# Optimization experiments

Measured on AMD Instinct MI355X. Metric: run time of the kernel, lower is better.

Reference implementation:

```python
import jax, jax.numpy as jnp
import numpy as np

D_MODEL = 256
NHEAD = 8
DK = D_MODEL // NHEAD
EDGE_FEAT_DIM = 7
N_NODES = 2048
N_EDGES = 65536
LN_EPS = 1e-5


def _ln(x, g, b):
    mu = jnp.mean(x, axis=-1, keepdims=True)
    var = jnp.mean(jnp.square(x - mu), axis=-1, keepdims=True)
    return (x - mu) * jax.lax.rsqrt(var + LN_EPS) * g + b


def setup_inputs() -> dict:
    key = jax.random.key(0)
    ks = jax.random.split(key, 16)
    d, h2 = D_MODEL, 2 * D_MODEL
    s = 0.02
    inp = {
        "h": jax.random.normal(ks[0], (N_NODES, d), jnp.float32),
        "edge_attr": jax.random.normal(ks[1], (N_EDGES, EDGE_FEAT_DIM), jnp.float32),
        # weights stored as (in, out): y = x @ W + b (matches torch Linear math)
        "Wq": s * jax.random.normal(ks[2], (d, d), jnp.float32),
        "bq": jnp.zeros((d,), jnp.float32),
        "Wk": s * jax.random.normal(ks[3], (d, d), jnp.float32),
        "bk": jnp.zeros((d,), jnp.float32),
        "Wv": s * jax.random.normal(ks[4], (d, d), jnp.float32),
        "bv": jnp.zeros((d,), jnp.float32),
        "Wo": s * jax.random.normal(ks[5], (d, d), jnp.float32),
        "bo": jnp.zeros((d,), jnp.float32),
        "We": s * jax.random.normal(ks[6], (EDGE_FEAT_DIM, NHEAD), jnp.float32),
        "be": jnp.zeros((NHEAD,), jnp.float32),
        "ln1_g": jnp.ones((d,), jnp.float32),
        "ln1_b": jnp.zeros((d,), jnp.float32),
        "fln_g": jnp.ones((d,), jnp.float32),
        "fln_b": jnp.zeros((d,), jnp.float32),
        "W1": s * jax.random.normal(ks[7], (d, h2), jnp.float32),
        "b1": jnp.zeros((h2,), jnp.float32),
        "W2": s * jax.random.normal(ks[8], (h2, d), jnp.float32),
        "b2": jnp.zeros((d,), jnp.float32),
        "edge_index": jax.random.randint(ks[9], (2, N_EDGES), 0, N_NODES, jnp.int64 if jax.config.jax_enable_x64 else jnp.int32),
    }
    return inp


def reference(h, edge_attr, Wq, bq, Wk, bk, Wv, bv, Wo, bo, We, be,
              ln1_g, ln1_b, fln_g, fln_b, W1, b1, W2, b2, edge_index):
    N = h.shape[0]
    res = h
    # edge bias scattered into dense (N, N, H) tensor
    eb = edge_attr @ We + be                                  # (E, H)
    attn_bias = jnp.zeros((N, N, NHEAD), h.dtype).at[edge_index[0], edge_index[1]].set(eb)
    Q = (h @ Wq + bq).reshape(N, NHEAD, DK)
    K = (h @ Wk + bk).reshape(N, NHEAD, DK)
    V = (h @ Wv + bv).reshape(N, NHEAD, DK)
    scores = jnp.einsum('nhd,mhd->nmh', Q, K) / jnp.sqrt(jnp.float32(DK)) + attn_bias
    attn = jax.nn.softmax(scores, axis=1)                     # softmax over keys m
    out = jnp.einsum('nmh,mhd->nhd', attn, V).reshape(N, D_MODEL)
    out = out @ Wo + bo
    h1 = _ln(res + out, ln1_g, ln1_b)
    ffn = jax.nn.gelu(_ln(h1, fln_g, fln_b) @ W1 + b1, approximate=False) @ W2 + b2
    return h1 + ffn
```

## Files before the change

### kernel.cpp

```cpp
#include <hip/hip_runtime.h>
#include <math.h>

#define NN 2048
#define NE 65536
#define DM 256
#define NH 8
#define DKH 32
#define CAP 128
#define TM2 128
#define SPLIT 4

typedef __attribute__((ext_vector_type(8))) short bf16x8;
typedef __attribute__((ext_vector_type(4))) float f32x4;

#define WAVE_LDS_SYNC() __asm__ volatile("s_waitcnt lgkmcnt(0)" ::: "memory")

__device__ __forceinline__ unsigned short f2b(float f) {
    unsigned u = __float_as_uint(f);
    unsigned r = (u + 0x7FFFu + ((u >> 16) & 1u)) >> 16;
    return (unsigned short)r;
}
__device__ __forceinline__ float b2f(unsigned short s) {
    return __uint_as_float(((unsigned)s) << 16);
}
__device__ __forceinline__ unsigned pk2(float a, float b) {
    unsigned ua = __float_as_uint(a) + 0x8000u;
    unsigned ub = __float_as_uint(b) + 0x8000u;
    return (ua >> 16) | (ub & 0xFFFF0000u);
}

__global__ __launch_bounds__(256) void prep_all_kernel(
    const float* __restrict__ Wq, const float* __restrict__ Wk,
    const float* __restrict__ Wv, const float* __restrict__ Wo,
    const float* __restrict__ W1, const float* __restrict__ W2,
    const float* __restrict__ ea, const float* __restrict__ We,
    const float* __restrict__ be, const int* __restrict__ ei,
    unsigned short* __restrict__ Wqkvt, unsigned short* __restrict__ Wot,
    unsigned short* __restrict__ W1t, unsigned short* __restrict__ W2t,
    float* __restrict__ eb, int* __restrict__ cnt, int* __restrict__ lst)
{
    int b = blockIdx.x;
    if (b < 2048) {
        int i = b * 256 + threadIdx.x;
        if (i < 196608) {
            int n = i >> 8, k = i & 255;
            const float* W = (n < 256) ? Wq : (n < 512) ? Wk : Wv;
            Wqkvt[i] = f2b(W[k * 256 + (n & 255)]);
        } else if (i < 262144) {
            int j = i - 196608;
            int n = j >> 8, k = j & 255;
            Wot[j] = f2b(Wo[k * 256 + n]);
        } else if (i < 393216) {
            int j = i - 262144;
            int n = j >> 8, k = j & 255;
            W1t[j] = f2b(W1[(size_t)k * 512 + n]);
        } else {
            int j = i - 393216;
            int n = j >> 9, k = j & 511;
            W2t[j] = f2b(W2[(size_t)k * 256 + n]);
        }
    } else {
        int e = (b - 2048) * 256 + threadIdx.x;
        float acc[NH];
#pragma unroll
        for (int hh = 0; hh < NH; ++hh) acc[hh] = be[hh];
#pragma unroll
        for (int f = 0; f < 7; ++f) {
            float x = ea[e * 7 + f];
#pragma unroll
            for (int hh = 0; hh < NH; ++hh) acc[hh] = fmaf(x, We[f * NH + hh], acc[hh]);
        }
#pragma unroll
        for (int hh = 0; hh < NH; ++hh)
            eb[e * NH + hh] = acc[hh] * 1.44269504088896f;
        int s = ei[e];
        int p = atomicAdd(&cnt[s], 1);
        if (p < CAP) lst[s * CAP + p] = e;
    }
}

__global__ __launch_bounds__(128) void rowprep_kernel(
    const int* __restrict__ ei, const int* __restrict__ cnt,
    const int* __restrict__ lst, int* __restrict__ sortedDest,
    int* __restrict__ sortedE, int* __restrict__ rowOff)
{
    __shared__ int ds[CAP], es[CAP];
    __shared__ int bc[16], off[17];
    int n = blockIdx.x, t = threadIdx.x;
    int c = cnt[n]; if (c > CAP) c = CAP;
    if (t < 16) bc[t] = 0;
    int e = -1, d = -1;
    if (t < c) { e = lst[n * CAP + t]; d = ei[NE + e]; }
    ds[t] = d; es[t] = e;
    __syncthreads();
    bool win = (t < c);
    if (win) {
        for (int j = 0; j < c; ++j)
            if (ds[j] == d && es[j] > e) { win = false; break; }
    }
    int bkt = (d >= 0) ? (d >> 7) : 0;
    int pos = -1;
    if (win) pos = atomicAdd(&bc[bkt], 1);
    __syncthreads();
    if (t == 0) {
        int s = 0;
        for (int i = 0; i < 16; ++i) { off[i] = s; s += bc[i]; }
        off[16] = s;
    }
    __syncthreads();
    if (win) {
        int p = off[bkt] + pos;
        sortedDest[n * CAP + p] = d;
        sortedE[n * CAP + p] = e;
    }
    if (t < 17) rowOff[n * 17 + t] = off[t];
}

template <int EPI, int MT, int AF32>
__global__ __launch_bounds__(MT * 4) void gemm_bf16(
    const void* __restrict__ Av, const unsigned short* __restrict__ Bt,
    const float* __restrict__ bias0, const float* __restrict__ bias1,
    const float* __restrict__ bias2, const float* __restrict__ resid,
    void* __restrict__ out0, void* __restrict__ out1, void* __restrict__ out2,
    int M, int N, int K)
{
    __shared__ __align__(16) unsigned short As[MT][136];
    __shared__ __align__(16) unsigned short Bs[64][136];
    int tid = threadIdx.x;
    int wv = tid >> 6, l = tid & 63, l15 = l & 15, quad = l >> 4;
    int m0 = blockIdx.y * MT, n0 = blockIdx.x * 64;

    f32x4 acc[4];
#pragma unroll
    for (int i = 0; i < 4; ++i) acc[i] = (f32x4){0.f, 0.f, 0.f, 0.f};

    for (int k0 = 0; k0 < K; k0 += 128) {
        if (MT == 64) {
            int row = tid >> 2, cb = (tid & 3) * 32;
            if (AF32) {
                const float* ap = (const float*)Av + (size_t)(m0 + row) * K + k0 + cb;
#pragma unroll
                for (int i = 0; i < 4; ++i) {
                    float4 f0 = *(const float4*)(ap + i * 8);
                    float4 f1 = *(const float4*)(ap + i * 8 + 4);
                    uint4 pk = { pk2(f0.x, f0.y), pk2(f0.z, f0.w),
                                 pk2(f1.x, f1.y), pk2(f1.z, f1.w) };
                    *(uint4*)&As[row][cb + i * 8] = pk;
                }
            } else {
                const unsigned short* ap =
                    (const unsigned short*)Av + (size_t)(m0 + row) * K + k0 + cb;
#pragma unroll
                for (int i = 0; i < 4; ++i)
                    *(uint4*)&As[row][cb + i * 8] = *(const uint4*)(ap + i * 8);
            }
            const unsigned short* bp = Bt + (size_t)(n0 + row) * K + k0 + cb;
#pragma unroll
            for (int i = 0; i < 4; ++i)
                *(uint4*)&Bs[row][cb + i * 8] = *(const uint4*)(bp + i * 8);
        } else {
            int rowa = tid >> 2, cba = (tid & 3) * 32;
            const unsigned short* ap =
                (const unsigned short*)Av + (size_t)(m0 + rowa) * K + k0 + cba;
#pragma unroll
            for (int i = 0; i < 4; ++i)
                *(uint4*)&As[rowa][cba + i * 8] = *(const uint4*)(ap + i * 8);
            int rowb = tid >> 1, cbb = (tid & 1) * 64;
            const unsigned short* bp = Bt + (size_t)(n0 + rowb) * K + k0 + cbb;
#pragma unroll
            for (int i = 0; i < 8; ++i)
                *(uint4*)&Bs[rowb][cbb + i * 8] = *(const uint4*)(bp + i * 8);
        }
        __syncthreads();
#pragma unroll
        for (int ks = 0; ks < 4; ++ks) {
            bf16x8 a = *(const bf16x8*)&As[wv * 16 + l15][ks * 32 + quad * 8];
#pragma unroll
            for (int nt = 0; nt < 4; ++nt) {
                bf16x8 b = *(const bf16x8*)&Bs[nt * 16 + l15][ks * 32 + quad * 8];
                acc[nt] = __builtin_amdgcn_mfma_f32_16x16x32_bf16(a, b, acc[nt], 0, 0, 0);
            }
        }
        __syncthreads();
    }

#pragma unroll
    for (int nt = 0; nt < 4; ++nt) {
        int colb = n0 + nt * 16;
        if (EPI == 2 && colb >= 512) {
            int n = colb + l15 - 512;
            float bv = bias2[n];
            uint2 pk = { pk2(acc[nt][0] + bv, acc[nt][1] + bv),
                         pk2(acc[nt][2] + bv, acc[nt][3] + bv) };
            *(uint2*)((unsigned short*)out2 + (size_t)n * NN + m0 + wv * 16 + quad * 4) = pk;
            continue;
        }
#pragma unroll
        for (int r = 0; r < 4; ++r) {
            int row = m0 + wv * 16 + quad * 4 + r;
            int col = colb + l15;
            float v = acc[nt][r];
            if (EPI == 0) {
                v += bias0[col];
                if (resid) v += resid[(size_t)row * N + col];
                ((float*)out0)[(size_t)row * N + col] = v;
            } else if (EPI == 1) {
                v += bias0[col];
                v = 0.5f * v * (1.0f + erff(v * 0.70710678118654752f));
                ((unsigned short*)out0)[(size_t)row * N + col] = f2b(v);
            } else {
                if (col < 256) {
                    v = (v + bias0[col]) * 0.2550348592f;
                    ((unsigned short*)out0)[(size_t)row * 256 + col] = f2b(v);
                } else {
                    v += bias1[col - 256];
                    ((unsigned short*)out1)[(size_t)row * 256 + col - 256] = f2b(v);
                }
            }
        }
    }
}

__global__ __launch_bounds__(256) void attn_mfma(
    const unsigned short* __restrict__ Qb, const unsigned short* __restrict__ Kb,
    const unsigned short* __restrict__ Vt, const float* __restrict__ eb,
    const int* __restrict__ sortedDest, const int* __restrict__ sortedE,
    const int* __restrict__ rowOff,
    float* __restrict__ accD, float* __restrict__ lD)
{
    __shared__ __align__(16) unsigned short Ks[TM2][40];
    __shared__ __align__(16) unsigned short Vs[32][TM2 + 8];
    __shared__ __align__(16) unsigned short Pn[4][16][TM2 + 16];
    int h = blockIdx.y, tid = threadIdx.x;
    int wv = tid >> 6, l = tid & 63, l15 = l & 15, quad = l >> 4;
    int n0 = blockIdx.x * 64 + wv * 16;
    int mz = blockIdx.z;

    bf16x8 aq = *(const bf16x8*)(Qb + (size_t)(n0 + l15) * DM + h * 32 + quad * 8);

    f32x4 oacc[2];
    oacc[0] = (f32x4){0.f, 0.f, 0.f, 0.f};
    oacc[1] = (f32x4){0.f, 0.f, 0.f, 0.f};
    float lacc = 0.f;
    float dreg = 0.f;
    const unsigned short* Vth = Vt + (size_t)h * 32 * NN;

    int r16 = l >> 2, sub = l & 3;
    int frow = n0 + r16;

    for (int t = 0; t < NN / (TM2 * SPLIT); ++t) {
        int m0 = (mz * (NN / SPLIT)) + t * TM2;
        int ti = m0 >> 7;
        {
            int r = tid >> 1, kc = (tid & 1) * 16;
            const unsigned short* ks = Kb + (size_t)(m0 + r) * DM + h * 32 + kc;
            *(uint4*)&Ks[r][kc]     = *(const uint4*)(ks);
            *(uint4*)&Ks[r][kc + 8] = *(const uint4*)(ks + 8);
            int d = tid >> 3, mc = (tid & 7) * 16;
            const unsigned short* vs = Vth + (size_t)d * NN + m0 + mc;
            *(uint4*)&Vs[d][mc]     = *(const uint4*)(vs);
            *(uint4*)&Vs[d][mc + 8] = *(const uint4*)(vs + 8);
        }
        __syncthreads();
#pragma unroll
        for (int mt = 0; mt < TM2 / 16; ++mt) {
            bf16x8 ak = *(const bf16x8*)&Ks[mt * 16 + l15][quad * 8];
            f32x4 s = __builtin_amdgcn_mfma_f32_16x16x32_bf16(
                ak, aq, (f32x4){0.f, 0.f, 0.f, 0.f}, 0, 0, 0);
            float p0 = __builtin_amdgcn_exp2f(s[0]);
            float p1 = __builtin_amdgcn_exp2f(s[1]);
            float p2 = __builtin_amdgcn_exp2f(s[2]);
            float p3 = __builtin_amdgcn_exp2f(s[3]);
            lacc += (p0 + p1) + (p2 + p3);
            *(uint2*)&Pn[wv][l15][mt * 16 + quad * 4] =
                (uint2){pk2(p0, p1), pk2(p2, p3)};
        }
        WAVE_LDS_SYNC();
        {
            int o0 = rowOff[frow * 17 + ti];
            int o1 = rowOff[frow * 17 + ti + 1];
            for (int idx = o0 + sub; idx < o1; idx += 4) {
                int d = sortedDest[frow * CAP + idx] - m0;
                int e = sortedE[frow * CAP + idx];
                float expb = __builtin_amdgcn_exp2f(eb[e * NH + h]);
                float pold = b2f(Pn[wv][r16][d]);
                Pn[wv][r16][d] = f2b(pold * expb);
                dreg += pold * (expb - 1.0f);
            }
        }
        WAVE_LDS_SYNC();
#pragma unroll
        for (int kc = 0; kc < TM2 / 32; ++kc) {
            bf16x8 ap = *(const bf16x8*)&Pn[wv][l15][kc * 32 + quad * 8];
#pragma unroll
            for (int nt = 0; nt < 2; ++nt) {
                bf16x8 bv = *(const bf16x8*)&Vs[nt * 16 + l15][kc * 32 + quad * 8];
                oacc[nt] = __builtin_amdgcn_mfma_f32_16x16x32_bf16(ap, bv, oacc[nt], 0, 0, 0);
            }
        }
        __syncthreads();
    }

    lacc += __shfl_xor(lacc, 16);
    lacc += __shfl_xor(lacc, 32);
    dreg += __shfl_xor(dreg, 1);
    dreg += __shfl_xor(dreg, 2);
    float dtot = __shfl(dreg, l15 * 4);
    float* lDp = lD + (size_t)mz * NN * NH;
    if (l < 16)
        lDp[(size_t)(n0 + l) * NH + h] = lacc + dtot;
    float* aDp = accD + (size_t)mz * NN * DM;
#pragma unroll
    for (int nt = 0; nt < 2; ++nt)
#pragma unroll
        for (int r = 0; r < 4; ++r)
            aDp[(size_t)(n0 + quad * 4 + r) * DM + h * 32 + nt * 16 + l15] = oacc[nt][r];
}

__global__ __launch_bounds__(512) void tail_fused_kernel(
    const float* __restrict__ accD, const float* __restrict__ lD,
    const unsigned short* __restrict__ Wot, const float* __restrict__ bo,
    const float* __restrict__ h, const float* __restrict__ ln1g,
    const float* __restrict__ ln1b, const float* __restrict__ flng,
    const float* __restrict__ flnb,
    const unsigned short* __restrict__ W1t, const float* __restrict__ fb1,
    const unsigned short* __restrict__ W2t, const float* __restrict__ fb2,
    float* __restrict__ out)
{
    __shared__ float linv[16][8];
    __shared__ __align__(16) unsigned short As[16][264];
    __shared__ float Tt[16][264];
    __shared__ __align__(16) unsigned short X2s[16][264];
    __shared__ __align__(16) unsigned short F1s[16][520];
    int tid = threadIdx.x, m0 = blockIdx.x * 16;
    int wv = tid >> 6, l = tid & 63, l15 = l & 15, quad = l >> 4;

    if (tid < 128) {
        int r = tid >> 3, hh = tid & 7;
        float ls = 0.f;
#pragma unroll
        for (int s = 0; s < SPLIT; ++s)
            ls += lD[(size_t)s * NN * NH + (size_t)(m0 + r) * NH + hh];
        linv[r][hh] = 1.0f / ls;
    }
    __syncthreads();
    {
        int col = tid & 255, rh = tid >> 8;
#pragma unroll
        for (int ch = 0; ch < 8; ++ch) {
            int row = ch * 2 + rh;
            float o = 0.f;
#pragma unroll
            for (int s = 0; s < SPLIT; ++s)
                o += accD[(size_t)s * NN * DM + (size_t)(m0 + row) * DM + col];
            As[row][col] = f2b(o * linv[row][col >> 5]);
        }
    }
    __syncthreads();

    f32x4 acc[2];
    acc[0] = (f32x4){0.f, 0.f, 0.f, 0.f};
    acc[1] = (f32x4){0.f, 0.f, 0.f, 0.f};
#pragma unroll
    for (int k0 = 0; k0 < 256; k0 += 32) {
        bf16x8 a = *(const bf16x8*)&As[l15][k0 + quad * 8];
#pragma unroll
        for (int nt = 0; nt < 2; ++nt) {
            int row = wv * 32 + nt * 16 + l15;
            bf16x8 b = *(const bf16x8*)(Wot + (size_t)row * 256 + k0 + quad * 8);
            acc[nt] = __builtin_amdgcn_mfma_f32_16x16x32_bf16(a, b, acc[nt], 0, 0, 0);
        }
    }
#pragma unroll
    for (int nt = 0; nt < 2; ++nt)
#pragma unroll
        for (int r = 0; r < 4; ++r) {
            int row = quad * 4 + r, col = wv * 32 + nt * 16 + l15;
            Tt[row][col] = acc[nt][r] + bo[col] + h[(size_t)(m0 + row) * DM + col];
        }
    __syncthreads();

    if (tid < 256) {
        int rr = tid >> 4, l16 = tid & 15;
        float x[16];
#pragma unroll
        for (int j = 0; j < 16; ++j) x[j] = Tt[rr][l16 + 16 * j];
        float mu = 0.f;
#pragma unroll
        for (int j = 0; j < 16; ++j) mu += x[j];
#pragma unroll
        for (int off = 1; off < 16; off <<= 1) mu += __shfl_xor(mu, off);
        mu *= (1.0f / 256.0f);
        float var = 0.f;
#pragma unroll
        for (int j = 0; j < 16; ++j) { float d = x[j] - mu; var += d * d; }
#pragma unroll
        for (int off = 1; off < 16; off <<= 1) var += __shfl_xor(var, off);
        float rs = rsqrtf(var * (1.0f / 256.0f) + 1e-5f);
        float y[16]; float mu2 = 0.f;
#pragma unroll
        for (int j = 0; j < 16; ++j) {
            int c = l16 + 16 * j;
            y[j] = (x[j] - mu) * rs * ln1g[c] + ln1b[c];
            mu2 += y[j];
        }
#pragma unroll
        for (int off = 1; off < 16; off <<= 1) mu2 += __shfl_xor(mu2, off);
        mu2 *= (1.0f / 256.0f);
        float var2 = 0.f;
#pragma unroll
        for (int j = 0; j < 16; ++j) { float d = y[j] - mu2; var2 += d * d; }
#pragma unroll
        for (int off = 1; off < 16; off <<= 1) var2 += __shfl_xor(var2, off);
        float rs2 = rsqrtf(var2 * (1.0f / 256.0f) + 1e-5f);
#pragma unroll
        for (int j = 0; j < 16; ++j) {
            int c = l16 + 16 * j;
            Tt[rr][c] = y[j];
            X2s[rr][c] = f2b((y[j] - mu2) * rs2 * flng[c] + flnb[c]);
        }
    }
    __syncthreads();

    f32x4 acc1[4];
#pragma unroll
    for (int i = 0; i < 4; ++i) acc1[i] = (f32x4){0.f, 0.f, 0.f, 0.f};
#pragma unroll
    for (int k0 = 0; k0 < 256; k0 += 32) {
        bf16x8 a = *(const bf16x8*)&X2s[l15][k0 + quad * 8];
#pragma unroll
        for (int nt = 0; nt < 4; ++nt) {
            int row = wv * 64 + nt * 16 + l15;
            bf16x8 b = *(const bf16x8*)(W1t + (size_t)row * 256 + k0 + quad * 8);
            acc1[nt] = __builtin_amdgcn_mfma_f32_16x16x32_bf16(a, b, acc1[nt], 0, 0, 0);
        }
    }
#pragma unroll
    for (int nt = 0; nt < 4; ++nt)
#pragma unroll
        for (int r = 0; r < 4; ++r) {
            int row = quad * 4 + r, col = wv * 64 + nt * 16 + l15;
            float v = acc1[nt][r] + fb1[col];
            v = 0.5f * v * (1.0f + erff(v * 0.70710678118654752f));
            F1s[row][col] = f2b(v);
        }
    __syncthreads();

    f32x4 acc2[2];
    acc2[0] = (f32x4){0.f, 0.f, 0.f, 0.f};
    acc2[1] = (f32x4){0.f, 0.f, 0.f, 0.f};
#pragma unroll
    for (int k0 = 0; k0 < 512; k0 += 32) {
        bf16x8 a = *(const bf16x8*)&F1s[l15][k0 + quad * 8];
#pragma unroll
        for (int nt = 0; nt < 2; ++nt) {
            int row = wv * 32 + nt * 16 + l15;
            bf16x8 b = *(const bf16x8*)(W2t + (size_t)row * 512 + k0 + quad * 8);
            acc2[nt] = __builtin_amdgcn_mfma_f32_16x16x32_bf16(a, b, acc2[nt], 0, 0, 0);
        }
    }
#pragma unroll
    for (int nt = 0; nt < 2; ++nt)
#pragma unroll
        for (int r = 0; r < 4; ++r) {
            int row = quad * 4 + r, col = wv * 32 + nt * 16 + l15;
            out[(size_t)(m0 + row) * DM + col] = acc2[nt][r] + fb2[col] + Tt[row][col];
        }
}

extern "C" void kernel_launch(void* const* d_in, const int* in_sizes, int n_in,
                              void* d_out, int out_size, void* d_ws, size_t ws_size,
                              hipStream_t stream)
{
    const float* h    = (const float*)d_in[0];
    const float* ea   = (const float*)d_in[1];
    const float* Wq   = (const float*)d_in[2];
    const float* bq   = (const float*)d_in[3];
    const float* Wk   = (const float*)d_in[4];
    const float* bk   = (const float*)d_in[5];
    const float* Wv   = (const float*)d_in[6];
    const float* bv   = (const float*)d_in[7];
    const float* Wo   = (const float*)d_in[8];
    const float* bo   = (const float*)d_in[9];
    const float* We   = (const float*)d_in[10];
    const float* be   = (const float*)d_in[11];
    const float* ln1g = (const float*)d_in[12];
    const float* ln1b = (const float*)d_in[13];
    const float* flng = (const float*)d_in[14];
    const float* flnb = (const float*)d_in[15];
    const float* W1   = (const float*)d_in[16];
    const float* b1   = (const float*)d_in[17];
    const float* W2   = (const float*)d_in[18];
    const float* b2   = (const float*)d_in[19];
    const int*   ei   = (const int*)d_in[20];
    float* out = (float*)d_out;

    char* p = (char*)d_ws;
    float* eb   = (float*)p;           p += (size_t)NE * NH * 4;
    int*   cnt  = (int*)p;             p += (size_t)NN * 4;
    int*   lst  = (int*)p;             p += (size_t)NN * CAP * 4;
    int*   sD   = (int*)p;             p += (size_t)NN * CAP * 4;
    int*   sE   = (int*)p;             p += (size_t)NN * CAP * 4;
    int*   rOff = (int*)p;             p += (size_t)NN * 17 * 4;
    unsigned short* Wqkvt = (unsigned short*)p; p += (size_t)768 * 256 * 2;
    unsigned short* Wot   = (unsigned short*)p; p += (size_t)256 * 256 * 2;
    unsigned short* W1t   = (unsigned short*)p; p += (size_t)512 * 256 * 2;
    unsigned short* W2t   = (unsigned short*)p; p += (size_t)256 * 512 * 2;
    unsigned short* Qb    = (unsigned short*)p; p += (size_t)NN * DM * 2;
    unsigned short* Kb    = (unsigned short*)p; p += (size_t)NN * DM * 2;
    unsigned short* Vt    = (unsigned short*)p; p += (size_t)NN * DM * 2;
    float* accD = (float*)p;           p += (size_t)SPLIT * NN * DM * 4;
    float* lD   = (float*)p;           p += (size_t)SPLIT * NN * NH * 4;

    hipMemsetAsync(cnt, 0, (size_t)NN * 4, stream);
    prep_all_kernel<<<2048 + NE / 256, 256, 0, stream>>>(
        Wq, Wk, Wv, Wo, W1, W2, ea, We, be, ei,
        Wqkvt, Wot, W1t, W2t, eb, cnt, lst);
    rowprep_kernel<<<NN, 128, 0, stream>>>(ei, cnt, lst, sD, sE, rOff);

    gemm_bf16<2, 64, 1><<<dim3(768 / 64, NN / 64), 256, 0, stream>>>(
        h, Wqkvt, bq, bk, bv, nullptr, Qb, Kb, Vt, NN, 768, 256);

    attn_mfma<<<dim3(NN / 64, NH, SPLIT), 256, 0, stream>>>(
        Qb, Kb, Vt, eb, sD, sE, rOff, accD, lD);

    tail_fused_kernel<<<NN / 16, 512, 0, stream>>>(
        accD, lD, Wot, bo, h, ln1g, ln1b, flng, flnb,
        W1t, b1, W2t, b2, out);
}
```

Measured before the change: 173.8 us.

## Tile weight transposes via LDS, pre-convert h to bf16, head-major Q/K layout

Weight transposition in the prep kernel moves from one-element-per-thread strided reads to 64x64 LDS-tiled transposes, cutting the block count and making the global accesses coalesced. The prep kernel also converts h to bf16 once, so the QKV GEMM reads bf16 input (template flag changed) instead of converting fp32 itself. Q and K are written in head-major [head][node][32] layout, so the attention kernel loads contiguous 64-byte rows per head instead of strided slices of 512-byte rows. This adds a workspace buffer and relies on the GEMM variant with flag 0 accepting bf16 input correctly.

Result: faster. 166.7 us (-4.1%).

```diff
diff --git a/kernel.cpp b/kernel.cpp
--- a/kernel.cpp
+++ b/kernel.cpp
@@ -29,38 +29,69 @@
     return (ua >> 16) | (ub & 0xFFFF0000u);
 }
 
+__device__ __forceinline__ void transpose_tile(
+    const float* __restrict__ src, int srcStride, int nc0, int k0s,
+    unsigned short* __restrict__ dst, int dstK, int n0d, int tid)
+{
+    __shared__ unsigned short T[64][66];
+    int tx = tid & 63, ty = tid >> 6;
+#pragma unroll
+    for (int r = 0; r < 16; ++r) {
+        int kk = ty + r * 4;
+        T[tx][kk] = f2b(src[(size_t)(k0s + kk) * srcStride + nc0 + tx]);
+    }
+    __syncthreads();
+#pragma unroll
+    for (int r = 0; r < 16; ++r) {
+        int nn = ty + r * 4;
+        dst[(size_t)(n0d + nn) * dstK + k0s + tx] = T[nn][tx];
+    }
+}
+
 __global__ __launch_bounds__(256) void prep_all_kernel(
     const float* __restrict__ Wq, const float* __restrict__ Wk,
     const float* __restrict__ Wv, const float* __restrict__ Wo,
     const float* __restrict__ W1, const float* __restrict__ W2,
-    const float* __restrict__ ea, const float* __restrict__ We,
-    const float* __restrict__ be, const int* __restrict__ ei,
+    const float* __restrict__ h, const float* __restrict__ ea,
+    const float* __restrict__ We, const float* __restrict__ be,
+    const int* __restrict__ ei,
     unsigned short* __restrict__ Wqkvt, unsigned short* __restrict__ Wot,
     unsigned short* __restrict__ W1t, unsigned short* __restrict__ W2t,
+    unsigned short* __restrict__ hb,
     float* __restrict__ eb, int* __restrict__ cnt, int* __restrict__ lst)
 {
     int b = blockIdx.x;
-    if (b < 2048) {
-        int i = b * 256 + threadIdx.x;
-        if (i < 196608) {
-            int n = i >> 8, k = i & 255;
-            const float* W = (n < 256) ? Wq : (n < 512) ? Wk : Wv;
-            Wqkvt[i] = f2b(W[k * 256 + (n & 255)]);
-        } else if (i < 262144) {
-            int j = i - 196608;
-            int n = j >> 8, k = j & 255;
-            Wot[j] = f2b(Wo[k * 256 + n]);
-        } else if (i < 393216) {
-            int j = i - 262144;
-            int n = j >> 8, k = j & 255;
-            W1t[j] = f2b(W1[(size_t)k * 512 + n]);
+    if (b < 128) {
+        const float* src; int srcStride, nc0, k0s, dstK, n0d;
+        unsigned short* dst;
+        if (b < 48) {
+            int tn = b >> 2, tk = b & 3, n0 = tn * 64;
+            src = (n0 < 256) ? Wq : (n0 < 512) ? Wk : Wv;
+            srcStride = 256; nc0 = n0 & 255; k0s = tk * 64;
+            dst = Wqkvt; dstK = 256; n0d = n0;
+        } else if (b < 64) {
+            int t = b - 48, tn = t >> 2, tk = t & 3;
+            src = Wo; srcStride = 256; nc0 = tn * 64; k0s = tk * 64;
+            dst = Wot; dstK = 256; n0d = tn * 64;
+        } else if (b < 96) {
+            int t = b - 64, tn = t >> 2, tk = t & 3;
+            src = W1; srcStride = 512; nc0 = tn * 64; k0s = tk * 64;
+            dst = W1t; dstK = 256; n0d = tn * 64;
         } else {
-            int j = i - 393216;
-            int n = j >> 9, k = j & 511;
-            W2t[j] = f2b(W2[(size_t)k * 256 + n]);
-        }
+            int t = b - 96, tn = t >> 3, tk = t & 7;
+            src = W2; srcStride = 256; nc0 = tn * 64; k0s = tk * 64;
+            dst = W2t; dstK = 512; n0d = tn * 64;
+        }
+        transpose_tile(src, srcStride, nc0, k0s, dst, dstK, n0d, threadIdx.x);
+    } else if (b < 384) {
+        int j = ((b - 128) * 256 + threadIdx.x) * 8;
+        const float* hp = h + j;
+        float4 f0 = *(const float4*)hp, f1 = *(const float4*)(hp + 4);
+        uint4 pk = { pk2(f0.x, f0.y), pk2(f0.z, f0.w),
+                     pk2(f1.x, f1.y), pk2(f1.z, f1.w) };
+        *(uint4*)(hb + j) = pk;
     } else {
-        int e = (b - 2048) * 256 + threadIdx.x;
+        int e = (b - 384) * 256 + threadIdx.x;
         float acc[NH];
 #pragma unroll
         for (int hh = 0; hh < NH; ++hh) acc[hh] = be[hh];
@@ -211,10 +242,13 @@
             } else {
                 if (col < 256) {
                     v = (v + bias0[col]) * 0.2550348592f;
-                    ((unsigned short*)out0)[(size_t)row * 256 + col] = f2b(v);
+                    ((unsigned short*)out0)[(size_t)(col >> 5) * (NN * 32)
+                        + (size_t)row * 32 + (col & 31)] = f2b(v);
                 } else {
-                    v += bias1[col - 256];
-                    ((unsigned short*)out1)[(size_t)row * 256 + col - 256] = f2b(v);
+                    int kc = col - 256;
+                    v += bias1[kc];
+                    ((unsigned short*)out1)[(size_t)(kc >> 5) * (NN * 32)
+                        + (size_t)row * 32 + (kc & 31)] = f2b(v);
                 }
             }
         }
@@ -236,7 +270,9 @@
     int n0 = blockIdx.x * 64 + wv * 16;
     int mz = blockIdx.z;
 
-    bf16x8 aq = *(const bf16x8*)(Qb + (size_t)(n0 + l15) * DM + h * 32 + quad * 8);
+    const unsigned short* Qh = Qb + (size_t)h * NN * 32;
+    const unsigned short* Kh = Kb + (size_t)h * NN * 32;
+    bf16x8 aq = *(const bf16x8*)(Qh + (size_t)(n0 + l15) * 32 + quad * 8);
 
     f32x4 oacc[2];
     oacc[0] = (f32x4){0.f, 0.f, 0.f, 0.f};
@@ -253,7 +289,7 @@
         int ti = m0 >> 7;
         {
             int r = tid >> 1, kc = (tid & 1) * 16;
-            const unsigned short* ks = Kb + (size_t)(m0 + r) * DM + h * 32 + kc;
+            const unsigned short* ks = Kh + (size_t)(m0 + r) * 32 + kc;
             *(uint4*)&Ks[r][kc]     = *(const uint4*)(ks);
             *(uint4*)&Ks[r][kc + 8] = *(const uint4*)(ks + 8);
             int d = tid >> 3, mc = (tid & 7) * 16;
@@ -506,6 +542,7 @@
     unsigned short* Wot   = (unsigned short*)p; p += (size_t)256 * 256 * 2;
     unsigned short* W1t   = (unsigned short*)p; p += (size_t)512 * 256 * 2;
     unsigned short* W2t   = (unsigned short*)p; p += (size_t)256 * 512 * 2;
+    unsigned short* hb    = (unsigned short*)p; p += (size_t)NN * DM * 2;
     unsigned short* Qb    = (unsigned short*)p; p += (size_t)NN * DM * 2;
     unsigned short* Kb    = (unsigned short*)p; p += (size_t)NN * DM * 2;
     unsigned short* Vt    = (unsigned short*)p; p += (size_t)NN * DM * 2;
@@ -513,13 +550,13 @@
     float* lD   = (float*)p;           p += (size_t)SPLIT * NN * NH * 4;
 
     hipMemsetAsync(cnt, 0, (size_t)NN * 4, stream);
-    prep_all_kernel<<<2048 + NE / 256, 256, 0, stream>>>(
-        Wq, Wk, Wv, Wo, W1, W2, ea, We, be, ei,
-        Wqkvt, Wot, W1t, W2t, eb, cnt, lst);
+    prep_all_kernel<<<384 + NE / 256, 256, 0, stream>>>(
+        Wq, Wk, Wv, Wo, W1, W2, h, ea, We, be, ei,
+        Wqkvt, Wot, W1t, W2t, hb, eb, cnt, lst);
     rowprep_kernel<<<NN, 128, 0, stream>>>(ei, cnt, lst, sD, sE, rOff);
 
-    gemm_bf16<2, 64, 1><<<dim3(768 / 64, NN / 64), 256, 0, stream>>>(
-        h, Wqkvt, bq, bk, bv, nullptr, Qb, Kb, Vt, NN, 768, 256);
+    gemm_bf16<2, 64, 0><<<dim3(768 / 64, NN / 64), 256, 0, stream>>>(
+        hb, Wqkvt, bq, bk, bv, nullptr, Qb, Kb, Vt, NN, 768, 256);
 
     attn_mfma<<<dim3(NN / 64, NH, SPLIT), 256, 0, stream>>>(
         Qb, Kb, Vt, eb, sD, sE, rOff, accD, lD);
```
